# Optimization experiments

Measured on AMD Instinct MI355X. Metric: run time of the kernel, lower is better.

The kernel has to match this reference:

```python
import jax, jax.numpy as jnp
import numpy as np

N = 1024
DIM = 128
HEADS = 8
DK = DIM // HEADS
EDIM = 16
EPS = 1e-5
NEG = -10000.0


def _lin(k, din, dout):
    return jax.random.normal(k, (din, dout), jnp.float32) * (1.0 / np.sqrt(din))


def setup_inputs() -> dict:
    key = jax.random.key(0)
    ks = jax.random.split(key, 10)
    mask = jax.random.randint(ks[2], (N, N), 0, 2).astype(bool)
    mask = mask | jnp.eye(N, dtype=bool)  # self-loops always valid
    return {
        "x": jax.random.normal(ks[0], (N, DIM), jnp.float32),
        "edge_feat": jax.random.normal(ks[1], (N, N, EDIM), jnp.float32),
        "mask": mask,
        "Wq": _lin(ks[3], DIM, DIM), "bq": jnp.zeros((DIM,), jnp.float32),
        "Wk": _lin(ks[4], DIM, DIM), "bk": jnp.zeros((DIM,), jnp.float32),
        "Wv": _lin(ks[5], DIM, DIM), "bv": jnp.zeros((DIM,), jnp.float32),
        "Wae": _lin(ks[6], EDIM, HEADS), "bae": jnp.zeros((HEADS,), jnp.float32),
        "Wve": _lin(ks[7], EDIM, DIM), "bve": jnp.zeros((DIM,), jnp.float32),
        "Wo": _lin(ks[8], DIM, DIM), "bo": jnp.zeros((DIM,), jnp.float32),
        "gamma": jnp.ones((DIM,), jnp.float32),
        "beta": jnp.zeros((DIM,), jnp.float32),
    }


def reference(x, edge_feat, mask, Wq, bq, Wk, bk, Wv, bv, Wae, bae, Wve, bve, Wo, bo, gamma, beta):
    n, dim = x.shape
    heads = bae.shape[0]
    dk = dim // heads
    # pre-LayerNorm
    mu = jnp.mean(x, axis=-1, keepdims=True)
    var = jnp.mean(jnp.square(x - mu), axis=-1, keepdims=True)
    h = (x - mu) * jax.lax.rsqrt(var + EPS) * gamma + beta
    q = (h @ Wq + bq).reshape(n, heads, dk)
    k = (h @ Wk + bk).reshape(n, heads, dk)
    v = (h @ Wv + bv).reshape(n, heads, dk)
    # attention logits with per-edge additive bias: (n, m, heads)
    att = jnp.einsum('nhd,mhd->nmh', q, k) / np.sqrt(dk).astype(np.float32)
    att = att + edge_feat @ Wae + bae
    att = jnp.where(mask[..., None], att, NEG)
    alpha = jax.nn.softmax(att, axis=1)  # softmax over source nodes m
    # edge-conditioned values: msg_{nm} = v_m + U(e_{nm})
    edge_val = (edge_feat @ Wve + bve).reshape(n, n, heads, dk)
    out = jnp.einsum('nmh,mhd->nhd', alpha, v) + jnp.einsum('nmh,nmhd->nhd', alpha, edge_val)
    out = out.reshape(n, dim) @ Wo + bo
    return x + out
```

## Files before the change

kernel.cpp:

```cpp
#include <hip/hip_runtime.h>
#include <hip/hip_bf16.h>

#define NNODE 1024
#define DIM 128
#define HEADS 8
#define DK 16
#define EDIM 16
#define BN 8
#define MSPLIT 16
#define MRANGE (NNODE / MSPLIT)
#define NJ (MRANGE / 8)
#define LOG2E 1.44269504f

__global__ __launch_bounds__(384)
void ln_qkv_kernel(const float* __restrict__ x,
                   const float* __restrict__ Wq, const float* __restrict__ bq,
                   const float* __restrict__ Wk, const float* __restrict__ bk,
                   const float* __restrict__ Wv, const float* __restrict__ bv,
                   const float* __restrict__ gamma, const float* __restrict__ beta,
                   float* __restrict__ qg, float* __restrict__ kg, float* __restrict__ vg) {
    const int n = blockIdx.x;
    const int t = threadIdx.x;
    __shared__ float hrow[DIM];
    __shared__ float part[4];

    float xv = 0.f;
    if (t < 128) {
        xv = x[n * DIM + t];
        float v = xv;
        #pragma unroll
        for (int off = 32; off >= 1; off >>= 1) v += __shfl_xor(v, off);
        if ((t & 63) == 0) part[t >> 6] = v;
    }
    __syncthreads();
    const float mu = (part[0] + part[1]) * (1.0f / DIM);
    const float dx = xv - mu;
    if (t < 128) {
        float v = dx * dx;
        #pragma unroll
        for (int off = 32; off >= 1; off >>= 1) v += __shfl_xor(v, off);
        if ((t & 63) == 0) part[2 + (t >> 6)] = v;
    }
    __syncthreads();
    if (t < 128) {
        const float var = (part[2] + part[3]) * (1.0f / DIM);
        hrow[t] = dx * rsqrtf(var + 1e-5f) * gamma[t] + beta[t];
    }
    __syncthreads();

    const int which = t >> 7;
    const int col = t & 127;
    const float* W = (which == 0) ? Wq : (which == 1) ? Wk : Wv;
    const float* b = (which == 0) ? bq : (which == 1) ? bk : bv;
    float* o       = (which == 0) ? qg : (which == 1) ? kg : vg;
    float acc = b[col];
    #pragma unroll 16
    for (int i = 0; i < DIM; ++i) acc = fmaf(hrow[i], W[i * DIM + col], acc);
    o[n * DIM + col] = acc;
}

__global__ __launch_bounds__(256, 2)
void attn_kernel(const float* __restrict__ qg, const float* __restrict__ kg,
                 const float* __restrict__ vg, const float* __restrict__ ef,
                 const int* __restrict__ mask,
                 const float* __restrict__ Wae, const float* __restrict__ bae,
                 float* __restrict__ acc) {
    const int t = threadIdx.x;
    const int s  = t >> 5;
    const int np = (t >> 3) & 3;
    const int h  = t & 7;
    const int wid = t >> 6, lane = t & 63;
    const int bx = blockIdx.x;
    const int n0 = (bx >> 4) * BN;
    const int mb = (bx & 15) * MRANGE;

    __shared__ float red2[2 * BN * HEADS * 33];

    float qreg[2][DK];
    #pragma unroll
    for (int hf = 0; hf < 2; ++hf) {
        const float* qp = qg + (size_t)(n0 + np + 4 * hf) * DIM + h * DK;
        #pragma unroll
        for (int d4 = 0; d4 < 4; ++d4) {
            const float4 qv = *(const float4*)(qp + d4 * 4);
            qreg[hf][d4 * 4 + 0] = qv.x; qreg[hf][d4 * 4 + 1] = qv.y;
            qreg[hf][d4 * 4 + 2] = qv.z; qreg[hf][d4 * 4 + 3] = qv.w;
        }
    }
    float waec[EDIM];
    #pragma unroll
    for (int e = 0; e < EDIM; ++e) waec[e] = Wae[e * HEADS + h] * LOG2E;
    const float baeh = bae[h] * LOG2E;

    float sl[2] = {0.f, 0.f};
    float accv[2][DK], accT[2][EDIM];
    #pragma unroll
    for (int hf = 0; hf < 2; ++hf) {
        #pragma unroll
        for (int d = 0; d < DK; ++d) accv[hf][d] = 0.f;
        #pragma unroll
        for (int e = 0; e < EDIM; ++e) accT[hf][e] = 0.f;
    }

    #pragma unroll 2
    for (int j = 0; j < NJ; ++j) {
        const int gm = mb + j * 8 + s;
        float kk[DK], vv[DK];
        const float* kp = kg + (size_t)gm * DIM + h * DK;
        const float* vp = vg + (size_t)gm * DIM + h * DK;
        #pragma unroll
        for (int d4 = 0; d4 < 4; ++d4) {
            const float4 k4 = *(const float4*)(kp + d4 * 4);
            kk[d4 * 4 + 0] = k4.x; kk[d4 * 4 + 1] = k4.y;
            kk[d4 * 4 + 2] = k4.z; kk[d4 * 4 + 3] = k4.w;
            const float4 v4 = *(const float4*)(vp + d4 * 4);
            vv[d4 * 4 + 0] = v4.x; vv[d4 * 4 + 1] = v4.y;
            vv[d4 * 4 + 2] = v4.z; vv[d4 * 4 + 3] = v4.w;
        }
        #pragma unroll
        for (int hf = 0; hf < 2; ++hf) {
            const int n = np + 4 * hf;
            const float* ep = ef + ((size_t)(n0 + n) * NNODE + gm) * EDIM;
            float efv[EDIM];
            #pragma unroll
            for (int e4 = 0; e4 < 4; ++e4) {
                const float4 ev = *(const float4*)(ep + e4 * 4);
                efv[e4 * 4 + 0] = ev.x; efv[e4 * 4 + 1] = ev.y;
                efv[e4 * 4 + 2] = ev.z; efv[e4 * 4 + 3] = ev.w;
            }
            const int mk = mask[(size_t)(n0 + n) * NNODE + gm];
            float bias = baeh, dot = 0.f;
            #pragma unroll
            for (int e = 0; e < EDIM; ++e) bias = fmaf(efv[e], waec[e], bias);
            #pragma unroll
            for (int d = 0; d < DK; ++d) dot = fmaf(qreg[hf][d], kk[d], dot);
            const float lg = fmaf(dot, 0.25f * LOG2E, bias);
            const float p = mk ? __builtin_amdgcn_exp2f(lg) : 0.f;
            sl[hf] += p;
            #pragma unroll
            for (int d = 0; d < DK; ++d) accv[hf][d] = fmaf(p, vv[d], accv[hf][d]);
            #pragma unroll
            for (int e = 0; e < EDIM; ++e) accT[hf][e] = fmaf(p, efv[e], accT[hf][e]);
        }
    }

    #pragma unroll
    for (int hf = 0; hf < 2; ++hf) {
        sl[hf] += __shfl_xor(sl[hf], 32);
        #pragma unroll
        for (int d = 0; d < DK; ++d) accv[hf][d] += __shfl_xor(accv[hf][d], 32);
        #pragma unroll
        for (int e = 0; e < EDIM; ++e) accT[hf][e] += __shfl_xor(accT[hf][e], 32);
    }
    float* redA = red2;
    float* redB = red2 + BN * HEADS * 33;
    if (lane < 32 && wid < 2) {
        float* base = (wid == 0) ? redA : redB;
        #pragma unroll
        for (int hf = 0; hf < 2; ++hf) {
            float* rp = base + ((np + 4 * hf) * 8 + h) * 33;
            rp[0] = sl[hf];
            #pragma unroll
            for (int d = 0; d < DK; ++d) rp[1 + d] = accv[hf][d];
            #pragma unroll
            for (int e = 0; e < EDIM; ++e) rp[17 + e] = accT[hf][e];
        }
    }
    __syncthreads();
    if (lane < 32 && wid >= 2) {
        float* base = (wid == 2) ? redA : redB;
        #pragma unroll
        for (int hf = 0; hf < 2; ++hf) {
            float* rp = base + ((np + 4 * hf) * 8 + h) * 33;
            rp[0] += sl[hf];
            #pragma unroll
            for (int d = 0; d < DK; ++d) rp[1 + d] += accv[hf][d];
            #pragma unroll
            for (int e = 0; e < EDIM; ++e) rp[17 + e] += accT[hf][e];
        }
    }
    __syncthreads();
    for (int u = t; u < BN * HEADS * 33; u += 256)
        atomicAdd(&acc[(size_t)n0 * HEADS * 33 + u], redA[u] + redB[u]);
}

__global__ __launch_bounds__(128)
void final_kernel(const float* __restrict__ acc,
                  const float* __restrict__ Wve, const float* __restrict__ bve,
                  const float* __restrict__ x,
                  const float* __restrict__ Wo, const float* __restrict__ bo,
                  float* __restrict__ out) {
    const int n = blockIdx.x, t = threadIdx.x;
    __shared__ float ab[HEADS * 33];
    __shared__ float orow[DIM];
    for (int u = t; u < HEADS * 33; u += 128) ab[u] = acc[(size_t)n * HEADS * 33 + u];
    __syncthreads();
    const int col = t, hh = col >> 4, dd = col & 15;
    const float slv = ab[hh * 33];
    float acc2 = 0.f;
    #pragma unroll
    for (int e = 0; e < EDIM; ++e) acc2 = fmaf(ab[hh * 33 + 17 + e], Wve[e * DIM + col], acc2);
    orow[col] = (ab[hh * 33 + 1 + dd] + acc2) / slv + bve[col];
    __syncthreads();
    float o = bo[col] + x[(size_t)n * DIM + col];
    #pragma unroll 16
    for (int i = 0; i < DIM; ++i) o = fmaf(orow[i], Wo[i * DIM + col], o);
    out[(size_t)n * DIM + col] = o;
}

extern "C" void kernel_launch(void* const* d_in, const int* in_sizes, int n_in,
                              void* d_out, int out_size, void* d_ws, size_t ws_size,
                              hipStream_t stream) {
    const float* x     = (const float*)d_in[0];
    const float* ef    = (const float*)d_in[1];
    const int*   mask  = (const int*)d_in[2];
    const float* Wq    = (const float*)d_in[3];
    const float* bq    = (const float*)d_in[4];
    const float* Wk    = (const float*)d_in[5];
    const float* bk    = (const float*)d_in[6];
    const float* Wv    = (const float*)d_in[7];
    const float* bv    = (const float*)d_in[8];
    const float* Wae   = (const float*)d_in[9];
    const float* bae   = (const float*)d_in[10];
    const float* Wve   = (const float*)d_in[11];
    const float* bve   = (const float*)d_in[12];
    const float* Wo    = (const float*)d_in[13];
    const float* bo    = (const float*)d_in[14];
    const float* gamma = (const float*)d_in[15];
    const float* beta  = (const float*)d_in[16];

    float* ws = (float*)d_ws;
    float* accb = ws;
    float* qg   = ws + 270336;
    float* kg   = qg + (size_t)NNODE * DIM;
    float* vg   = kg + (size_t)NNODE * DIM;

    hipMemsetAsync(accb, 0, (size_t)NNODE * HEADS * 33 * sizeof(float), stream);
    ln_qkv_kernel<<<NNODE, 384, 0, stream>>>(x, Wq, bq, Wk, bk, Wv, bv, gamma, beta, qg, kg, vg);
    attn_kernel<<<(NNODE / BN) * MSPLIT, 256, 0, stream>>>(qg, kg, vg, ef, mask, Wae, bae, accb);
    final_kernel<<<NNODE, 128, 0, stream>>>(accb, Wve, bve, x, Wo, bo, (float*)d_out);
}
```

Baseline: 191.1 us.

## Compact mask into per-row index lists and skip masked edges in attention

Adds a mask-scan kernel that uses wave ballots to build, for each destination node, a compact list of valid source indices and a count. The attention kernel then iterates only over valid sources, gathering k, v and edge features by index, so it skips the roughly half of edge-feature loads and compute that the mask zeroes out. The thread mapping changes to one node per 32-thread group with shuffle reductions and direct global atomics, which replaces the shared-memory reduction. The cost is an extra kernel launch, irregular gathered loads, and more atomics per block.

After: 315.7 us. 1.65x slower.

```diff
diff --git a/kernel.cpp b/kernel.cpp
--- a/kernel.cpp
+++ b/kernel.cpp
@@ -7,9 +7,7 @@
 #define DK 16
 #define EDIM 16
 #define BN 8
-#define MSPLIT 16
-#define MRANGE (NNODE / MSPLIT)
-#define NJ (MRANGE / 8)
+#define MSPLIT 8
 #define LOG2E 1.44269504f
 
 __global__ __launch_bounds__(384)
@@ -59,32 +57,47 @@
     o[n * DIM + col] = acc;
 }
 
+__global__ __launch_bounds__(64)
+void mask_scan_kernel(const int* __restrict__ mask,
+                      unsigned short* __restrict__ idx, int* __restrict__ cnt) {
+    const int n = blockIdx.x;
+    const int l = threadIdx.x;
+    int base = 0;
+    #pragma unroll 1
+    for (int c = 0; c < NNODE / 64; ++c) {
+        const int m = c * 64 + l;
+        const bool v = mask[(size_t)n * NNODE + m] != 0;
+        const unsigned long long b = __ballot(v);
+        const int pre = __popcll(b & ((1ull << l) - 1ull));
+        if (v) idx[(size_t)n * NNODE + base + pre] = (unsigned short)m;
+        base += __popcll(b);
+    }
+    if (l == 0) cnt[n] = base;
+}
+
 __global__ __launch_bounds__(256, 2)
 void attn_kernel(const float* __restrict__ qg, const float* __restrict__ kg,
                  const float* __restrict__ vg, const float* __restrict__ ef,
-                 const int* __restrict__ mask,
+                 const unsigned short* __restrict__ idx, const int* __restrict__ cnt,
                  const float* __restrict__ Wae, const float* __restrict__ bae,
                  float* __restrict__ acc) {
     const int t = threadIdx.x;
-    const int s  = t >> 5;
-    const int np = (t >> 3) & 3;
-    const int h  = t & 7;
-    const int wid = t >> 6, lane = t & 63;
+    const int h = t & 7;
+    const int mslot = (t >> 3) & 3;
+    const int nl = t >> 5;
     const int bx = blockIdx.x;
-    const int n0 = (bx >> 4) * BN;
-    const int mb = (bx & 15) * MRANGE;
-
-    __shared__ float red2[2 * BN * HEADS * 33];
-
-    float qreg[2][DK];
-    #pragma unroll
-    for (int hf = 0; hf < 2; ++hf) {
-        const float* qp = qg + (size_t)(n0 + np + 4 * hf) * DIM + h * DK;
+    const int n0 = (bx >> 3) * BN;
+    const int ms = bx & 7;
+    const int n = n0 + nl;
+
+    float qreg[DK];
+    {
+        const float* qp = qg + (size_t)n * DIM + h * DK;
         #pragma unroll
         for (int d4 = 0; d4 < 4; ++d4) {
             const float4 qv = *(const float4*)(qp + d4 * 4);
-            qreg[hf][d4 * 4 + 0] = qv.x; qreg[hf][d4 * 4 + 1] = qv.y;
-            qreg[hf][d4 * 4 + 2] = qv.z; qreg[hf][d4 * 4 + 3] = qv.w;
+            qreg[d4 * 4 + 0] = qv.x; qreg[d4 * 4 + 1] = qv.y;
+            qreg[d4 * 4 + 2] = qv.z; qreg[d4 * 4 + 3] = qv.w;
         }
     }
     float waec[EDIM];
@@ -92,22 +105,27 @@
     for (int e = 0; e < EDIM; ++e) waec[e] = Wae[e * HEADS + h] * LOG2E;
     const float baeh = bae[h] * LOG2E;
 
-    float sl[2] = {0.f, 0.f};
-    float accv[2][DK], accT[2][EDIM];
-    #pragma unroll
-    for (int hf = 0; hf < 2; ++hf) {
-        #pragma unroll
-        for (int d = 0; d < DK; ++d) accv[hf][d] = 0.f;
-        #pragma unroll
-        for (int e = 0; e < EDIM; ++e) accT[hf][e] = 0.f;
-    }
-
-    #pragma unroll 2
-    for (int j = 0; j < NJ; ++j) {
-        const int gm = mb + j * 8 + s;
-        float kk[DK], vv[DK];
-        const float* kp = kg + (size_t)gm * DIM + h * DK;
-        const float* vp = vg + (size_t)gm * DIM + h * DK;
+    const int c = cnt[n];
+    const unsigned short* ip = idx + (size_t)n * NNODE;
+    const float* efn = ef + (size_t)n * NNODE * EDIM;
+
+    float sl = 0.f, accv[DK], accT[EDIM];
+    #pragma unroll
+    for (int d = 0; d < DK; ++d) accv[d] = 0.f;
+    #pragma unroll
+    for (int e = 0; e < EDIM; ++e) accT[e] = 0.f;
+
+    int i = ms * 4 + mslot;
+    int m = (i < c) ? (int)ip[i] : 0;
+    #pragma unroll 1
+    while (i < c) {
+        const int inext = i + 32;
+        const int mnext = (inext < c) ? (int)ip[inext] : 0;
+
+        const float* kp = kg + (size_t)m * DIM + h * DK;
+        const float* vp = vg + (size_t)m * DIM + h * DK;
+        const float* ep = efn + (size_t)m * EDIM;
+        float kk[DK], vv[DK], efv[EDIM];
         #pragma unroll
         for (int d4 = 0; d4 < 4; ++d4) {
             const float4 k4 = *(const float4*)(kp + d4 * 4);
@@ -116,72 +134,41 @@
             const float4 v4 = *(const float4*)(vp + d4 * 4);
             vv[d4 * 4 + 0] = v4.x; vv[d4 * 4 + 1] = v4.y;
             vv[d4 * 4 + 2] = v4.z; vv[d4 * 4 + 3] = v4.w;
+            const float4 e4 = *(const float4*)(ep + d4 * 4);
+            efv[d4 * 4 + 0] = e4.x; efv[d4 * 4 + 1] = e4.y;
+            efv[d4 * 4 + 2] = e4.z; efv[d4 * 4 + 3] = e4.w;
         }
-        #pragma unroll
-        for (int hf = 0; hf < 2; ++hf) {
-            const int n = np + 4 * hf;
-            const float* ep = ef + ((size_t)(n0 + n) * NNODE + gm) * EDIM;
-            float efv[EDIM];
-            #pragma unroll
-            for (int e4 = 0; e4 < 4; ++e4) {
-                const float4 ev = *(const float4*)(ep + e4 * 4);
-                efv[e4 * 4 + 0] = ev.x; efv[e4 * 4 + 1] = ev.y;
-                efv[e4 * 4 + 2] = ev.z; efv[e4 * 4 + 3] = ev.w;
-            }
-            const int mk = mask[(size_t)(n0 + n) * NNODE + gm];
-            float bias = baeh, dot = 0.f;
-            #pragma unroll
-            for (int e = 0; e < EDIM; ++e) bias = fmaf(efv[e], waec[e], bias);
-            #pragma unroll
-            for (int d = 0; d < DK; ++d) dot = fmaf(qreg[hf][d], kk[d], dot);
-            const float lg = fmaf(dot, 0.25f * LOG2E, bias);
-            const float p = mk ? __builtin_amdgcn_exp2f(lg) : 0.f;
-            sl[hf] += p;
-            #pragma unroll
-            for (int d = 0; d < DK; ++d) accv[hf][d] = fmaf(p, vv[d], accv[hf][d]);
-            #pragma unroll
-            for (int e = 0; e < EDIM; ++e) accT[hf][e] = fmaf(p, efv[e], accT[hf][e]);
-        }
-    }
-
-    #pragma unroll
-    for (int hf = 0; hf < 2; ++hf) {
-        sl[hf] += __shfl_xor(sl[hf], 32);
-        #pragma unroll
-        for (int d = 0; d < DK; ++d) accv[hf][d] += __shfl_xor(accv[hf][d], 32);
-        #pragma unroll
-        for (int e = 0; e < EDIM; ++e) accT[hf][e] += __shfl_xor(accT[hf][e], 32);
-    }
-    float* redA = red2;
-    float* redB = red2 + BN * HEADS * 33;
-    if (lane < 32 && wid < 2) {
-        float* base = (wid == 0) ? redA : redB;
-        #pragma unroll
-        for (int hf = 0; hf < 2; ++hf) {
-            float* rp = base + ((np + 4 * hf) * 8 + h) * 33;
-            rp[0] = sl[hf];
-            #pragma unroll
-            for (int d = 0; d < DK; ++d) rp[1 + d] = accv[hf][d];
-            #pragma unroll
-            for (int e = 0; e < EDIM; ++e) rp[17 + e] = accT[hf][e];
-        }
-    }
-    __syncthreads();
-    if (lane < 32 && wid >= 2) {
-        float* base = (wid == 2) ? redA : redB;
-        #pragma unroll
-        for (int hf = 0; hf < 2; ++hf) {
-            float* rp = base + ((np + 4 * hf) * 8 + h) * 33;
-            rp[0] += sl[hf];
-            #pragma unroll
-            for (int d = 0; d < DK; ++d) rp[1 + d] += accv[hf][d];
-            #pragma unroll
-            for (int e = 0; e < EDIM; ++e) rp[17 + e] += accT[hf][e];
-        }
-    }
-    __syncthreads();
-    for (int u = t; u < BN * HEADS * 33; u += 256)
-        atomicAdd(&acc[(size_t)n0 * HEADS * 33 + u], redA[u] + redB[u]);
+        float bias = baeh, dot = 0.f;
+        #pragma unroll
+        for (int e = 0; e < EDIM; ++e) bias = fmaf(efv[e], waec[e], bias);
+        #pragma unroll
+        for (int d = 0; d < DK; ++d) dot = fmaf(qreg[d], kk[d], dot);
+        const float p = __builtin_amdgcn_exp2f(fmaf(dot, 0.25f * LOG2E, bias));
+        sl += p;
+        #pragma unroll
+        for (int d = 0; d < DK; ++d) accv[d] = fmaf(p, vv[d], accv[d]);
+        #pragma unroll
+        for (int e = 0; e < EDIM; ++e) accT[e] = fmaf(p, efv[e], accT[e]);
+
+        i = inext; m = mnext;
+    }
+
+    #pragma unroll
+    for (int off = 8; off <= 16; off <<= 1) {
+        sl += __shfl_xor(sl, off);
+        #pragma unroll
+        for (int d = 0; d < DK; ++d) accv[d] += __shfl_xor(accv[d], off);
+        #pragma unroll
+        for (int e = 0; e < EDIM; ++e) accT[e] += __shfl_xor(accT[e], off);
+    }
+    if (mslot == 0) {
+        float* ap = acc + ((size_t)n * HEADS + h) * 33;
+        atomicAdd(&ap[0], sl);
+        #pragma unroll
+        for (int d = 0; d < DK; ++d) atomicAdd(&ap[1 + d], accv[d]);
+        #pragma unroll
+        for (int e = 0; e < EDIM; ++e) atomicAdd(&ap[17 + e], accT[e]);
+    }
 }
 
 __global__ __launch_bounds__(128)
@@ -234,9 +221,13 @@
     float* qg   = ws + 270336;
     float* kg   = qg + (size_t)NNODE * DIM;
     float* vg   = kg + (size_t)NNODE * DIM;
+    unsigned short* idxb = (unsigned short*)(vg + (size_t)NNODE * DIM);
+    int* cntb = (int*)(idxb + (size_t)NNODE * NNODE);
 
     hipMemsetAsync(accb, 0, (size_t)NNODE * HEADS * 33 * sizeof(float), stream);
+    mask_scan_kernel<<<NNODE, 64, 0, stream>>>(mask, idxb, cntb);
     ln_qkv_kernel<<<NNODE, 384, 0, stream>>>(x, Wq, bq, Wk, bk, Wv, bv, gamma, beta, qg, kg, vg);
-    attn_kernel<<<(NNODE / BN) * MSPLIT, 256, 0, stream>>>(qg, kg, vg, ef, mask, Wae, bae, accb);
+    attn_kernel<<<(NNODE / BN) * MSPLIT, 256, 0, stream>>>(qg, kg, vg, ef, idxb, cntb,
+                                                          Wae, bae, accb);
     final_kernel<<<NNODE, 128, 0, stream>>>(accb, Wve, bve, x, Wo, bo, (float*)d_out);
 }
```
